# Performance work log

Hardware: AMD Instinct MI355X
Metric: run time of the kernel (lower is better)

Reference implementation:

```python
import jax, jax.numpy as jnp
import numpy as np

NEG_BIG = -9e15
ALPHA = 0.2  # LeakyReLU negative slope


def setup_inputs() -> dict:
    key = jax.random.key(0)
    k1, k2, k3, k4 = jax.random.split(key, 4)
    N, F_in, F_out = 8192, 256, 64
    inp = jax.random.normal(k1, (N, F_in), dtype=jnp.float32)
    adj = jax.random.randint(k2, (N, N), 0, 2, dtype=jnp.int32)
    W = jax.random.normal(k3, (F_in, F_out), dtype=jnp.float32) * 0.05
    a = jax.random.normal(k4, (2 * F_out, 1), dtype=jnp.float32) * 0.05
    return {"input": inp, "adj": adj, "W": W, "a": a}


def reference(input, adj, W, a):
    # h = X W : [N, F_out]
    h = input @ W
    F_out = W.shape[1]
    # a_input[i,j] = concat(h_i, h_j); a_input @ a = h@a1 broadcast over j + h@a2 broadcast over i.
    a1 = a[:F_out, 0]   # [F_out]
    a2 = a[F_out:, 0]   # [F_out]
    s1 = h @ a1         # [N]
    s2 = h @ a2         # [N]
    e = jax.nn.leaky_relu(s1[:, None] + s2[None, :], negative_slope=ALPHA)  # [N, N]
    att = jnp.where(adj > 0, e, jnp.float32(NEG_BIG))
    att = jax.nn.softmax(att, axis=1)
    # dropout is identity in eval mode (training=False)
    h_prime = att @ h   # [N, F_out]
    return jax.nn.elu(h_prime)
```

## Files before the change

### kernel.cpp

```cpp
#include <hip/hip_runtime.h>
#include <hip/hip_bf16.h>

typedef __bf16 bf16_t;
typedef __attribute__((ext_vector_type(8))) __bf16 bf16x8;
typedef __attribute__((ext_vector_type(4))) __bf16 bf16x4;
typedef __attribute__((ext_vector_type(4))) float floatx4;
typedef __attribute__((ext_vector_type(4))) int intx4;

#define NN 8192
#define FIN 256
#define FOUT 64
#define GAT_ALPHA 0.2f
#define NSLICE 16
#define JS (NN / NSLICE)
#define NCH (JS / 64)

typedef const __attribute__((address_space(1))) void gv_t;
typedef __attribute__((address_space(3))) void lv_t;
#define GLOAD16(gp, lp) \
    __builtin_amdgcn_global_load_lds((gv_t*)(gp), (lv_t*)(lp), 16, 0, 0)

__global__ __launch_bounds__(256) void gat_h_kernel(
    const float* __restrict__ input,
    const float* __restrict__ W,
    const float* __restrict__ a,
    bf16_t* __restrict__ hT,
    float* __restrict__ s1g, float* __restrict__ e1g, float* __restrict__ f1g,
    float* __restrict__ s2g, float* __restrict__ e2g, float* __restrict__ f2g)
{
    alignas(16) __shared__ bf16_t in_lds[32][264];
    alignas(16) __shared__ bf16_t wt_lds[64][264];
    __shared__ float h_lds[32][65];

    const int t  = threadIdx.x;
    const int i0 = blockIdx.x * 32;

    #pragma unroll
    for (int v = 0; v < 8; v++) {
        int u  = v * 256 + t;
        int i  = u >> 6;
        int k4 = (u & 63) * 4;
        floatx4 x = *(const floatx4*)(input + (size_t)(i0 + i) * FIN + k4);
        bf16x4 b;
        #pragma unroll
        for (int e = 0; e < 4; e++) b[e] = (bf16_t)x[e];
        *(bf16x4*)(&in_lds[i][k4]) = b;
    }
    #pragma unroll
    for (int v = 0; v < 16; v++) {
        int u  = v * 256 + t;
        int k  = u >> 4;
        int f4 = (u & 15) * 4;
        floatx4 wv = *(const floatx4*)(W + k * FOUT + f4);
        #pragma unroll
        for (int e = 0; e < 4; e++) wt_lds[f4 + e][k] = (bf16_t)wv[e];
    }
    __syncthreads();

    const int wave = t >> 6;
    const int lane = t & 63;
    const int i16  = (wave & 1) * 16;
    const int f32  = (wave >> 1) * 32;
    const int lm   = lane & 15;
    const int lq   = lane >> 4;

    floatx4 acc0 = {0.f, 0.f, 0.f, 0.f};
    floatx4 acc1 = {0.f, 0.f, 0.f, 0.f};
    #pragma unroll
    for (int ks = 0; ks < 8; ks++) {
        int ko = ks * 32 + lq * 8;
        bf16x8 af = *(const bf16x8*)(&in_lds[i16 + lm][ko]);
        bf16x8 b0 = *(const bf16x8*)(&wt_lds[f32 + lm][ko]);
        bf16x8 b1 = *(const bf16x8*)(&wt_lds[f32 + 16 + lm][ko]);
        acc0 = __builtin_amdgcn_mfma_f32_16x16x32_bf16(af, b0, acc0, 0, 0, 0);
        acc1 = __builtin_amdgcn_mfma_f32_16x16x32_bf16(af, b1, acc1, 0, 0, 0);
    }

    #pragma unroll
    for (int c = 0; c < 2; c++) {
        floatx4 acc = c ? acc1 : acc0;
        int f  = f32 + c * 16 + lm;
        int ib = i0 + i16 + lq * 4;
        bf16x4 hp;
        #pragma unroll
        for (int r = 0; r < 4; r++) hp[r] = (bf16_t)acc[r];
        *(bf16x4*)(hT + (size_t)f * NN + ib) = hp;
    }
    #pragma unroll
    for (int c = 0; c < 2; c++) {
        floatx4 acc = c ? acc1 : acc0;
        #pragma unroll
        for (int r = 0; r < 4; r++)
            h_lds[i16 + lq * 4 + r][f32 + c * 16 + lm] = acc[r];
    }
    __syncthreads();

    if (t < 64) {
        int r   = t & 31;
        int sel = t >> 5;
        const float* av = a + sel * FOUT;
        float s = 0.f;
        #pragma unroll 8
        for (int f = 0; f < FOUT; f++) s += h_lds[r][f] * av[f];
        int gi = i0 + r;
        float E = expf(s);
        float F = expf(GAT_ALPHA * s);
        if (sel == 0) { s1g[gi] = s; e1g[gi] = E; f1g[gi] = F; }
        else          { s2g[gi] = s; e2g[gi] = E; f2g[gi] = F; }
    }
}

__global__ __launch_bounds__(256, 4) void gat_att_kernel(
    const int* __restrict__ adj,
    const bf16_t* __restrict__ hT,
    const float* __restrict__ e1g, const float* __restrict__ f1g,
    const float* __restrict__ e2g, const float* __restrict__ f2g,
    float* __restrict__ pacc,
    float* __restrict__ prs)
{
    __shared__ int    adjL[2][32][64];
    alignas(16) __shared__ bf16_t htL[2][64][64];
    __shared__ float  e2l[JS], f2l[JS];

    const int t     = threadIdx.x;
    const int i0    = blockIdx.x * 32;
    const int slice = blockIdx.y;
    const int jbase = slice * JS;

    const int wave = t >> 6;
    const int lane = t & 63;
    const int lm   = lane & 15;
    const int lq   = lane >> 4;
    const int wm   = wave & 1;
    const int wf   = wave >> 1;
    const int xm   = lm & 7;

    {
        const float* src = (wave & 2) ? f2g : e2g;
        float*       dst = (wave & 2) ? f2l : e2l;
        int off = (wave & 1) * 256;
        GLOAD16(src + jbase + off + lane * 4, dst + off);
    }

    auto stage = [&](int b, int c) {
        const int jg = jbase + c * 64;
        #pragma unroll
        for (int h = 0; h < 2; h++) {
            int r0 = wave * 8 + h * 4;
            int i  = r0 + (lane >> 4);
            int gl = (lane & 15) ^ (i & 7);
            GLOAD16(adj + (size_t)(i0 + i) * NN + jg + gl * 4,
                    &adjL[b][r0][0]);
        }
        #pragma unroll
        for (int h = 0; h < 2; h++) {
            int f0 = wave * 16 + h * 8;
            int f  = f0 + (lane >> 3);
            int gl = (lane & 7) ^ (f & 7);
            GLOAD16(hT + (size_t)f * NN + jg + gl * 8,
                    &htL[b][f0][0]);
        }
    };

    stage(0, 0);
    stage(1, 1);

    const int   row = i0 + wm * 16 + lm;
    const float E1  = e1g[row];
    const float F1  = f1g[row];

    floatx4 acc0 = {0.f,0.f,0.f,0.f}, acc1 = {0.f,0.f,0.f,0.f};
    floatx4 accR = {0.f,0.f,0.f,0.f};
    bf16x8 ones;
    #pragma unroll
    for (int e = 0; e < 8; e++) ones[e] = (bf16_t)1.0f;

    #pragma unroll
    for (int c = 0; c < NCH; c++) {
        const int b = c & 1;
        if (c + 1 < NCH) asm volatile("s_waitcnt vmcnt(4)" ::: "memory");
        else             asm volatile("s_waitcnt vmcnt(0)" ::: "memory");
        __builtin_amdgcn_s_barrier();
        asm volatile("" ::: "memory");

        const char* aB = (const char*)&adjL[b][wm * 16 + lm][0];
        const char* hB = (const char*)&htL[b][0][0];
        const int   j0 = c * 64;
        #pragma unroll
        for (int ks = 0; ks < 2; ks++) {
            intx4 a0 = *(const intx4*)(aB + (((ks * 8 + lq * 2 + 0) ^ xm) << 4));
            intx4 a1 = *(const intx4*)(aB + (((ks * 8 + lq * 2 + 1) ^ xm) << 4));
            int jo = j0 + ks * 32 + lq * 8;
            floatx4 e2a = *(const floatx4*)(&e2l[jo]);
            floatx4 e2b = *(const floatx4*)(&e2l[jo + 4]);
            floatx4 f2a = *(const floatx4*)(&f2l[jo]);
            floatx4 f2b = *(const floatx4*)(&f2l[jo + 4]);
            bf16x8 frag;
            #pragma unroll
            for (int e = 0; e < 4; e++) {
                float w0 = fmaxf(E1 * e2a[e], F1 * f2a[e]);
                frag[e]     = (bf16_t)((a0[e] > 0) ? w0 : 0.f);
                float w1 = fmaxf(E1 * e2b[e], F1 * f2b[e]);
                frag[e + 4] = (bf16_t)((a1[e] > 0) ? w1 : 0.f);
            }
            int gh = ((ks * 4 + lq) ^ xm) << 4;
            bf16x8 b0 = *(const bf16x8*)(hB + (wf * 32 + lm) * 128 + gh);
            bf16x8 b1 = *(const bf16x8*)(hB + (wf * 32 + 16 + lm) * 128 + gh);
            acc0 = __builtin_amdgcn_mfma_f32_16x16x32_bf16(frag, b0, acc0, 0, 0, 0);
            acc1 = __builtin_amdgcn_mfma_f32_16x16x32_bf16(frag, b1, acc1, 0, 0, 0);
            if (wf == 0)
                accR = __builtin_amdgcn_mfma_f32_16x16x32_bf16(frag, ones, accR, 0, 0, 0);
        }

        asm volatile("" ::: "memory");
        __builtin_amdgcn_s_barrier();
        asm volatile("" ::: "memory");
        if (c + 2 < NCH) stage(b, c + 2);
    }

    if (wf == 0 && lm == 0) {
        #pragma unroll
        for (int r = 0; r < 4; r++)
            prs[(size_t)slice * NN + i0 + wm * 16 + lq * 4 + r] = accR[r];
    }

    float* pa = pacc + (size_t)slice * NN * FOUT
                     + (size_t)(i0 + wm * 16) * FOUT;
    #pragma unroll
    for (int ft = 0; ft < 2; ft++) {
        floatx4 acc = ft ? acc1 : acc0;
        #pragma unroll
        for (int r = 0; r < 4; r++)
            pa[(size_t)(lq * 4 + r) * FOUT + wf * 32 + ft * 16 + lm] = acc[r];
    }
}

__global__ __launch_bounds__(256) void gat_combine_kernel(
    const float* __restrict__ pacc,
    const float* __restrict__ prs,
    float* __restrict__ out)
{
    int idx = blockIdx.x * 256 + threadIdx.x;
    int i   = idx >> 4;
    floatx4 s = {0.f, 0.f, 0.f, 0.f};
    float rs  = 0.f;
    #pragma unroll
    for (int p = 0; p < NSLICE; p++) {
        floatx4 v = *(const floatx4*)(pacc + (size_t)p * NN * FOUT + (size_t)idx * 4);
        s += v;
        rs += prs[p * NN + i];
    }
    float rinv = (rs > 0.f) ? 1.0f / rs : 0.f;
    floatx4 r;
    #pragma unroll
    for (int e = 0; e < 4; e++) {
        float x = s[e] * rinv;
        r[e] = (x > 0.f) ? x : (expf(x) - 1.0f);
    }
    *(floatx4*)(out + (size_t)idx * 4) = r;
}

extern "C" void kernel_launch(void* const* d_in, const int* in_sizes, int n_in,
                              void* d_out, int out_size, void* d_ws, size_t ws_size,
                              hipStream_t stream) {
    const float* input = (const float*)d_in[0];
    const int*   adj   = (const int*)d_in[1];
    const float* W     = (const float*)d_in[2];
    const float* a     = (const float*)d_in[3];
    float*       out   = (float*)d_out;

    char* ws = (char*)d_ws;
    bf16_t* hT  = (bf16_t*)ws;
    float*  s1g = (float*)(ws + (1 << 20));
    float*  e1g = s1g + NN;
    float*  f1g = e1g + NN;
    float*  s2g = f1g + NN;
    float*  e2g = s2g + NN;
    float*  f2g = e2g + NN;
    float*  pacc = f2g + NN;
    float*  prs  = pacc + (size_t)NSLICE * NN * FOUT;

    gat_h_kernel<<<NN / 32, 256, 0, stream>>>(input, W, a, hT,
                                              s1g, e1g, f1g, s2g, e2g, f2g);
    dim3 gridB(NN / 32, NSLICE);
    gat_att_kernel<<<gridB, 256, 0, stream>>>(adj, hT, e1g, f1g, e2g, f2g,
                                              pacc, prs);
    gat_combine_kernel<<<NN * FOUT / 4 / 256, 256, 0, stream>>>(pacc, prs, out);
}
```

Baseline: 398.5 us.

## Pre-swizzle h into MFMA fragment layout and read it directly from global

The h kernel now writes h in a fragment-ready layout, so the attention kernel can load MFMA B operands straight from global memory and no longer stages h through LDS. The attention kernel uses 64-row blocks in which each wave owns all 64 output features, processes 128-column adjacency chunks, and splits the j range into 4 slices instead of 16. This shrinks the partial-sum buffer and the combine work, and drops the s1/s2 outputs. In exchange the kernel carries more accumulators per wave, runs at lower occupancy (launch bounds 2), uses a non-unrolled loop that issues the next stage at the top of each iteration, and depends on cache hits for the h reads.

```diff
diff --git a/kernel.cpp b/kernel.cpp
--- a/kernel.cpp
+++ b/kernel.cpp
@@ -11,9 +11,11 @@
 #define FIN 256
 #define FOUT 64
 #define GAT_ALPHA 0.2f
-#define NSLICE 16
+#define NSLICE 4
 #define JS (NN / NSLICE)
-#define NCH (JS / 64)
+#define JCH 128
+#define NCH (JS / JCH)
+#define IB 64
 
 typedef const __attribute__((address_space(1))) void gv_t;
 typedef __attribute__((address_space(3))) void lv_t;
@@ -24,9 +26,9 @@
     const float* __restrict__ input,
     const float* __restrict__ W,
     const float* __restrict__ a,
-    bf16_t* __restrict__ hT,
-    float* __restrict__ s1g, float* __restrict__ e1g, float* __restrict__ f1g,
-    float* __restrict__ s2g, float* __restrict__ e2g, float* __restrict__ f2g)
+    bf16_t* __restrict__ hTf,
+    float* __restrict__ e1g, float* __restrict__ f1g,
+    float* __restrict__ e2g, float* __restrict__ f2g)
 {
     alignas(16) __shared__ bf16_t in_lds[32][264];
     alignas(16) __shared__ bf16_t wt_lds[64][264];
@@ -76,15 +78,19 @@
         acc1 = __builtin_amdgcn_mfma_f32_16x16x32_bf16(af, b1, acc1, 0, 0, 0);
     }
 
-    #pragma unroll
-    for (int c = 0; c < 2; c++) {
-        floatx4 acc = c ? acc1 : acc0;
-        int f  = f32 + c * 16 + lm;
-        int ib = i0 + i16 + lq * 4;
-        bf16x4 hp;
-        #pragma unroll
-        for (int r = 0; r < 4; r++) hp[r] = (bf16_t)acc[r];
-        *(bf16x4*)(hT + (size_t)f * NN + ib) = hp;
+    {
+        const int jb  = i0 >> 5;
+        const int lqp = (i16 >> 3) + (lq >> 1);
+        const int e0  = (lq & 1) * 4;
+        #pragma unroll
+        for (int c = 0; c < 2; c++) {
+            floatx4 acc = c ? acc1 : acc0;
+            int ft = (f32 >> 4) + c;
+            bf16x4 hp;
+            #pragma unroll
+            for (int r = 0; r < 4; r++) hp[r] = (bf16_t)acc[r];
+            *(bf16x4*)(hTf + (size_t)(((jb * 4 + ft) * 64 + lqp * 16 + lm) * 8 + e0)) = hp;
+        }
     }
     #pragma unroll
     for (int c = 0; c < 2; c++) {
@@ -105,25 +111,24 @@
         int gi = i0 + r;
         float E = expf(s);
         float F = expf(GAT_ALPHA * s);
-        if (sel == 0) { s1g[gi] = s; e1g[gi] = E; f1g[gi] = F; }
-        else          { s2g[gi] = s; e2g[gi] = E; f2g[gi] = F; }
-    }
-}
-
-__global__ __launch_bounds__(256, 4) void gat_att_kernel(
+        if (sel == 0) { e1g[gi] = E; f1g[gi] = F; }
+        else          { e2g[gi] = E; f2g[gi] = F; }
+    }
+}
+
+__global__ __launch_bounds__(256, 2) void gat_att_kernel(
     const int* __restrict__ adj,
-    const bf16_t* __restrict__ hT,
+    const bf16_t* __restrict__ hTf,
     const float* __restrict__ e1g, const float* __restrict__ f1g,
     const float* __restrict__ e2g, const float* __restrict__ f2g,
     float* __restrict__ pacc,
     float* __restrict__ prs)
 {
-    __shared__ int    adjL[2][32][64];
-    alignas(16) __shared__ bf16_t htL[2][64][64];
-    __shared__ float  e2l[JS], f2l[JS];
+    __shared__ int   adjL[2][IB][JCH];
+    __shared__ float e2l[JS], f2l[JS];
 
     const int t     = threadIdx.x;
-    const int i0    = blockIdx.x * 32;
+    const int i0    = blockIdx.x * IB;
     const int slice = blockIdx.y;
     const int jbase = slice * JS;
 
@@ -131,66 +136,56 @@
     const int lane = t & 63;
     const int lm   = lane & 15;
     const int lq   = lane >> 4;
-    const int wm   = wave & 1;
-    const int wf   = wave >> 1;
-    const int xm   = lm & 7;
 
     {
-        const float* src = (wave & 2) ? f2g : e2g;
-        float*       dst = (wave & 2) ? f2l : e2l;
-        int off = (wave & 1) * 256;
-        GLOAD16(src + jbase + off + lane * 4, dst + off);
+        int o = wave * 512;
+        GLOAD16(e2g + jbase + o + lane * 4,       e2l + o);
+        GLOAD16(e2g + jbase + o + 256 + lane * 4, e2l + o + 256);
+        GLOAD16(f2g + jbase + o + lane * 4,       f2l + o);
+        GLOAD16(f2g + jbase + o + 256 + lane * 4, f2l + o + 256);
     }
 
     auto stage = [&](int b, int c) {
-        const int jg = jbase + c * 64;
-        #pragma unroll
-        for (int h = 0; h < 2; h++) {
-            int r0 = wave * 8 + h * 4;
-            int i  = r0 + (lane >> 4);
-            int gl = (lane & 15) ^ (i & 7);
-            GLOAD16(adj + (size_t)(i0 + i) * NN + jg + gl * 4,
-                    &adjL[b][r0][0]);
-        }
-        #pragma unroll
-        for (int h = 0; h < 2; h++) {
-            int f0 = wave * 16 + h * 8;
-            int f  = f0 + (lane >> 3);
-            int gl = (lane & 7) ^ (f & 7);
-            GLOAD16(hT + (size_t)f * NN + jg + gl * 8,
-                    &htL[b][f0][0]);
+        const int jg = jbase + c * JCH;
+        #pragma unroll
+        for (int h = 0; h < 8; h++) {
+            int r0 = wave * 16 + h * 2;
+            int r  = r0 + (lane >> 5);
+            int g  = (lane & 31) ^ (r & 7);
+            GLOAD16(adj + (size_t)(i0 + r) * NN + jg + g * 4, &adjL[b][r0][0]);
         }
     };
 
     stage(0, 0);
-    stage(1, 1);
-
-    const int   row = i0 + wm * 16 + lm;
+
+    const int   row = i0 + wave * 16 + lm;
     const float E1  = e1g[row];
     const float F1  = f1g[row];
 
     floatx4 acc0 = {0.f,0.f,0.f,0.f}, acc1 = {0.f,0.f,0.f,0.f};
+    floatx4 acc2 = {0.f,0.f,0.f,0.f}, acc3 = {0.f,0.f,0.f,0.f};
     floatx4 accR = {0.f,0.f,0.f,0.f};
     bf16x8 ones;
     #pragma unroll
     for (int e = 0; e < 8; e++) ones[e] = (bf16_t)1.0f;
 
-    #pragma unroll
     for (int c = 0; c < NCH; c++) {
-        const int b = c & 1;
-        if (c + 1 < NCH) asm volatile("s_waitcnt vmcnt(4)" ::: "memory");
-        else             asm volatile("s_waitcnt vmcnt(0)" ::: "memory");
+        if (c + 1 < NCH) {
+            stage((c + 1) & 1, c + 1);
+            asm volatile("s_waitcnt vmcnt(8)" ::: "memory");
+        } else {
+            asm volatile("s_waitcnt vmcnt(0)" ::: "memory");
+        }
         __builtin_amdgcn_s_barrier();
         asm volatile("" ::: "memory");
 
-        const char* aB = (const char*)&adjL[b][wm * 16 + lm][0];
-        const char* hB = (const char*)&htL[b][0][0];
-        const int   j0 = c * 64;
-        #pragma unroll
-        for (int ks = 0; ks < 2; ks++) {
-            intx4 a0 = *(const intx4*)(aB + (((ks * 8 + lq * 2 + 0) ^ xm) << 4));
-            intx4 a1 = *(const intx4*)(aB + (((ks * 8 + lq * 2 + 1) ^ xm) << 4));
-            int jo = j0 + ks * 32 + lq * 8;
+        const char* aB = (const char*)&adjL[c & 1][wave * 16 + lm][0];
+        #pragma unroll
+        for (int ks = 0; ks < 4; ks++) {
+            int g0 = ks * 8 + lq * 2;
+            intx4 a0 = *(const intx4*)(aB + (((g0    ) ^ (lm & 7)) << 4));
+            intx4 a1 = *(const intx4*)(aB + (((g0 + 1) ^ (lm & 7)) << 4));
+            int jo = c * JCH + ks * 32 + lq * 8;
             floatx4 e2a = *(const floatx4*)(&e2l[jo]);
             floatx4 e2b = *(const floatx4*)(&e2l[jo + 4]);
             floatx4 f2a = *(const floatx4*)(&f2l[jo]);
@@ -203,35 +198,39 @@
                 float w1 = fmaxf(E1 * e2b[e], F1 * f2b[e]);
                 frag[e + 4] = (bf16_t)((a1[e] > 0) ? w1 : 0.f);
             }
-            int gh = ((ks * 4 + lq) ^ xm) << 4;
-            bf16x8 b0 = *(const bf16x8*)(hB + (wf * 32 + lm) * 128 + gh);
-            bf16x8 b1 = *(const bf16x8*)(hB + (wf * 32 + 16 + lm) * 128 + gh);
+            const int jb = slice * (JS / 32) + c * 4 + ks;
+            const bf16_t* hb = hTf + (size_t)jb * 2048 + (size_t)lane * 8;
+            bf16x8 b0 = *(const bf16x8*)(hb);
+            bf16x8 b1 = *(const bf16x8*)(hb + 512);
+            bf16x8 b2 = *(const bf16x8*)(hb + 1024);
+            bf16x8 b3 = *(const bf16x8*)(hb + 1536);
             acc0 = __builtin_amdgcn_mfma_f32_16x16x32_bf16(frag, b0, acc0, 0, 0, 0);
             acc1 = __builtin_amdgcn_mfma_f32_16x16x32_bf16(frag, b1, acc1, 0, 0, 0);
-            if (wf == 0)
-                accR = __builtin_amdgcn_mfma_f32_16x16x32_bf16(frag, ones, accR, 0, 0, 0);
+            acc2 = __builtin_amdgcn_mfma_f32_16x16x32_bf16(frag, b2, acc2, 0, 0, 0);
+            acc3 = __builtin_amdgcn_mfma_f32_16x16x32_bf16(frag, b3, acc3, 0, 0, 0);
+            accR = __builtin_amdgcn_mfma_f32_16x16x32_bf16(frag, ones, accR, 0, 0, 0);
         }
 
         asm volatile("" ::: "memory");
         __builtin_amdgcn_s_barrier();
         asm volatile("" ::: "memory");
-        if (c + 2 < NCH) stage(b, c + 2);
-    }
-
-    if (wf == 0 && lm == 0) {
+    }
+
+    if (lm == 0) {
         #pragma unroll
         for (int r = 0; r < 4; r++)
-            prs[(size_t)slice * NN + i0 + wm * 16 + lq * 4 + r] = accR[r];
+            prs[(size_t)slice * NN + i0 + wave * 16 + lq * 4 + r] = accR[r];
     }
 
     float* pa = pacc + (size_t)slice * NN * FOUT
-                     + (size_t)(i0 + wm * 16) * FOUT;
-    #pragma unroll
-    for (int ft = 0; ft < 2; ft++) {
-        floatx4 acc = ft ? acc1 : acc0;
+                     + (size_t)(i0 + wave * 16) * FOUT;
+    #pragma unroll
+    for (int ft = 0; ft < 4; ft++) {
+        floatx4 acc = (ft == 0) ? acc0 : (ft == 1) ? acc1
+                    : (ft == 2) ? acc2 : acc3;
         #pragma unroll
         for (int r = 0; r < 4; r++)
-            pa[(size_t)(lq * 4 + r) * FOUT + wf * 32 + ft * 16 + lm] = acc[r];
+            pa[(size_t)(lq * 4 + r) * FOUT + ft * 16 + lm] = acc[r];
     }
 }
 
@@ -270,20 +269,18 @@
     float*       out   = (float*)d_out;
 
     char* ws = (char*)d_ws;
-    bf16_t* hT  = (bf16_t*)ws;
-    float*  s1g = (float*)(ws + (1 << 20));
-    float*  e1g = s1g + NN;
+    bf16_t* hTf = (bf16_t*)ws;
+    float*  e1g = (float*)(ws + (1 << 20));
     float*  f1g = e1g + NN;
-    float*  s2g = f1g + NN;
-    float*  e2g = s2g + NN;
+    float*  e2g = f1g + NN;
     float*  f2g = e2g + NN;
     float*  pacc = f2g + NN;
     float*  prs  = pacc + (size_t)NSLICE * NN * FOUT;
 
-    gat_h_kernel<<<NN / 32, 256, 0, stream>>>(input, W, a, hT,
-                                              s1g, e1g, f1g, s2g, e2g, f2g);
-    dim3 gridB(NN / 32, NSLICE);
-    gat_att_kernel<<<gridB, 256, 0, stream>>>(adj, hT, e1g, f1g, e2g, f2g,
+    gat_h_kernel<<<NN / 32, 256, 0, stream>>>(input, W, a, hTf,
+                                              e1g, f1g, e2g, f2g);
+    dim3 gridB(NN / IB, NSLICE);
+    gat_att_kernel<<<gridB, 256, 0, stream>>>(adj, hTf, e1g, f1g, e2g, f2g,
                                               pacc, prs);
     gat_combine_kernel<<<NN * FOUT / 4 / 256, 256, 0, stream>>>(pacc, prs, out);
 }
```

After: 393.1 us. About the same (-1.4%).
